# Kernel optimization log

Hardware: AMD Instinct MI355X
Metric: run time of the kernel (lower is better)

Reference implementation:

```python
import jax, jax.numpy as jnp
import numpy as np

N = 50000; E = 1600000; W = 12; CIN = 32; CMID = 32; COUT = 32; K = 2; KER = 3; DIL = 1


def setup_inputs() -> dict:
    key = jax.random.key(0)
    ks = jax.random.split(key, 6)
    x = jax.random.normal(ks[0], (W, N, CIN), jnp.float32)
    A = jax.random.randint(ks[1], (2, E), 0, N, jnp.int32)
    Ew = jax.random.uniform(ks[2], (E,), jnp.float32)
    Wcheb = jax.random.normal(ks[3], (W, K, CIN, CMID), jnp.float32) / np.sqrt(CIN)
    bcheb = jnp.zeros((W, CMID), jnp.float32)
    Wconv = jax.random.normal(ks[4], (COUT, CMID, KER), jnp.float32) / np.sqrt(CMID * KER)
    bconv = jnp.zeros((COUT,), jnp.float32)
    return dict(x=x, A=A, Ew=Ew, Wcheb=Wcheb, bcheb=bcheb, Wconv=Wconv, bconv=bconv, batch_size=1)


def _prop(x, src, dst, w_hat):
    # one sparse matvec with L_hat per timestep; x: [W, N, C]
    msg = x[:, src, :] * w_hat[None, :, None]                      # [W, E, C]
    agg = jax.ops.segment_sum(msg.transpose(1, 0, 2), dst, num_segments=x.shape[1])  # [N, W, C]
    return agg.transpose(1, 0, 2)                                  # [W, N, C]


def reference(x, A, Ew, Wcheb, bcheb, Wconv, bconv, batch_size):
    src, dst = A[0], A[1]
    # sym-normalized Laplacian with lambda_max=2: L_hat = -D^{-1/2} A D^{-1/2}
    deg = jax.ops.segment_sum(Ew, dst, num_segments=x.shape[1])
    dinv = jnp.where(deg > 0, jax.lax.rsqrt(jnp.maximum(deg, 1e-12)), 0.0)
    w_hat = -dinv[src] * Ew * dinv[dst]

    # Chebyshev recurrence (vectorized over all window_size graphs at once)
    Txs = [x, _prop(x, src, dst, w_hat)]
    for _ in range(Wcheb.shape[1] - 2):
        Txs.append(2.0 * _prop(Txs[-1], src, dst, w_hat) - Txs[-2])

    out = bcheb[:, None, :]                                        # [W, 1, CMID]
    for k, Txk in enumerate(Txs):
        out = out + jnp.einsum('wnc,wcd->wnd', Txk, Wcheb[:, k])   # per-timestep weights

    # temporal Conv1d over the window axis: nodes act as conv batch
    h = out.transpose(1, 2, 0)                                     # [N, CMID, W]
    pad = (KER // 2) * DIL
    h = jax.lax.conv_general_dilated(h, Wconv, (1,), [(pad, pad)], rhs_dilation=(DIL,),
                                     dimension_numbers=('NCH', 'OIH', 'NCH'))
    h = h + bconv[None, :, None]
    h = h.transpose(0, 2, 1)                                       # [N, W, COUT]
    h = jnp.where(h >= 0, h, 0.01 * h)                             # LeakyReLU; dropout p=0 is identity
    return h
```

## Files before the change

kernel.cpp:

```cpp
#include <hip/hip_runtime.h>

#define WW 12
#define CH 32
#define KERN 3
#define SBT 256
#define ROWB 384

typedef __attribute__((ext_vector_type(8))) short short8v;
typedef __attribute__((ext_vector_type(4))) short short4v;
typedef __attribute__((ext_vector_type(4))) float f32x4;

__device__ __forceinline__ unsigned short bf16rne(float v) {
  unsigned int u = __float_as_uint(v);
  return (unsigned short)((u + 0x7FFFu + ((u >> 16) & 1u)) >> 16);
}
__device__ __forceinline__ float bf16tof(unsigned int b) {
  return __uint_as_float(b << 16);
}

__device__ __forceinline__ unsigned char fp8e4m3(float x) {
  unsigned int u = __float_as_uint(x);
  unsigned int s = (u >> 24) & 0x80u;
  float ax = fabsf(x);
  if (ax >= 464.f) return (unsigned char)(s | 0x7E);
  if (ax < 0.015625f) {
    int m = __float2int_rn(ax * 512.f);
    return (unsigned char)(s | (unsigned)m);
  }
  unsigned int au = u & 0x7fffffffu;
  au += 0x7FFFFu + ((au >> 20) & 1u);
  int e = (int)(au >> 23) - 127 + 7;
  unsigned int m = (au >> 20) & 7u;
  if (e > 15 || (e == 15 && m == 7)) return (unsigned char)(s | 0x7E);
  return (unsigned char)(s | ((unsigned)e << 3) | m);
}

__device__ __forceinline__ void dec4fma(unsigned int u, float wh, float* acc) {
#if __has_builtin(__builtin_amdgcn_cvt_pk_f32_fp8)
  auto lo = __builtin_amdgcn_cvt_pk_f32_fp8((int)u, false);
  auto hi = __builtin_amdgcn_cvt_pk_f32_fp8((int)u, true);
  acc[0] = fmaf(wh, lo[0], acc[0]);
  acc[1] = fmaf(wh, lo[1], acc[1]);
  acc[2] = fmaf(wh, hi[0], acc[2]);
  acc[3] = fmaf(wh, hi[1], acc[3]);
#else
#pragma unroll
  for (int j = 0; j < 4; ++j) {
    unsigned int b = (u >> (8 * j)) & 0xffu;
    float f = __uint_as_float(((b & 0x80u) << 24) | ((b & 0x7fu) << 20)) * 0x1.0p120f;
    acc[j] = fmaf(wh, f, acc[j]);
  }
#endif
}

__global__ void rankpack_kernel(const int* __restrict__ dst, const float* __restrict__ Ew,
                                unsigned long long* __restrict__ degcnt,
                                unsigned short* __restrict__ rank,
                                const float* __restrict__ x, const float* __restrict__ Wcheb,
                                const float* __restrict__ Wconv,
                                unsigned short* __restrict__ xt, unsigned char* __restrict__ xq,
                                unsigned short* __restrict__ wb01, unsigned short* __restrict__ wbc,
                                int E, int N, int npackTot, int npx) {
  const int group = blockIdx.x / 7;
  const int slot = blockIdx.x % 7;
  if (slot == 6) {
    int base = group * 1024 + threadIdx.x;
#pragma unroll
    for (int u = 0; u < 4; ++u) {
      int e = base + u * 256;
      if (e < E) {
        unsigned int q = (unsigned int)__float2int_rn(Ew[e] * 33554432.f);
        unsigned long long old =
            atomicAdd(&degcnt[dst[e]], (1ULL << 32) | (unsigned long long)q);
        rank[e] = (unsigned short)(old >> 32);
      }
    }
    return;
  }
  int pid = group * 6 + slot;
  if (pid >= npackTot) return;
  if (pid < npx) {
    long long f = ((long long)pid * 256 + threadIdx.x) * 8;
    const long long T = (long long)WW * N * CH;
    if (f >= T) return;
    float4 v0 = *(const float4*)(x + f);
    float4 v1 = *(const float4*)(x + f + 4);
    int w = (int)(f / ((long long)N * CH));
    int rem = (int)(f - (long long)w * N * CH);
    int n = rem >> 5;
    int c = rem & 31;
    size_t o = (size_t)n * ROWB + w * CH + c;
    short4v h0, h1;
    h0[0] = (short)bf16rne(v0.x); h0[1] = (short)bf16rne(v0.y);
    h0[2] = (short)bf16rne(v0.z); h0[3] = (short)bf16rne(v0.w);
    h1[0] = (short)bf16rne(v1.x); h1[1] = (short)bf16rne(v1.y);
    h1[2] = (short)bf16rne(v1.z); h1[3] = (short)bf16rne(v1.w);
    *(short4v*)(xt + o) = h0;
    *(short4v*)(xt + o + 4) = h1;
    unsigned int q0 = (unsigned int)fp8e4m3(v0.x) | ((unsigned int)fp8e4m3(v0.y) << 8) |
                      ((unsigned int)fp8e4m3(v0.z) << 16) | ((unsigned int)fp8e4m3(v0.w) << 24);
    unsigned int q1 = (unsigned int)fp8e4m3(v1.x) | ((unsigned int)fp8e4m3(v1.y) << 8) |
                      ((unsigned int)fp8e4m3(v1.z) << 16) | ((unsigned int)fp8e4m3(v1.w) << 24);
    *(unsigned int*)(xq + o) = q0;
    *(unsigned int*)(xq + o + 4) = q1;
    return;
  }
  int id = (pid - npx) * 256 + threadIdx.x;
  if (id < 12 * 2 * 2 * 64 * 8) {
    int j = id & 7, l = (id >> 3) & 63, h = (id >> 9) & 1, m = (id >> 10) & 1, ww = id >> 11;
    int k = ((l >> 4) << 3) + j;
    int d = (l & 15) + (h << 4);
    wb01[id] = bf16rne(Wcheb[((size_t)(ww * 2 + m) * 32 + k) * 32 + d]);
  } else if (id < 24576 + 3 * 2 * 64 * 8) {
    int i2 = id - 24576;
    int j = i2 & 7, l = (i2 >> 3) & 63, h = (i2 >> 9) & 1, k = i2 >> 10;
    int c = ((l >> 4) << 3) + j;
    int o = (l & 15) + (h << 4);
    wbc[i2] = bf16rne(Wconv[((size_t)(o * 32 + c)) * 3 + k]);
  }
}

__global__ void scanA_kernel(const unsigned long long* __restrict__ degcnt,
                             int* __restrict__ bsum, int N) {
  __shared__ int red[SBT];
  int i = blockIdx.x * SBT + threadIdx.x;
  red[threadIdx.x] = (i < N) ? (int)(degcnt[i] >> 32) : 0;
  __syncthreads();
  for (int o = SBT / 2; o > 0; o >>= 1) {
    if (threadIdx.x < o) red[threadIdx.x] += red[threadIdx.x + o];
    __syncthreads();
  }
  if (threadIdx.x == 0) bsum[blockIdx.x] = red[0];
}

__global__ void scanB_kernel(int* __restrict__ bsum, int* __restrict__ rowptr,
                             int nb, int N) {
  __shared__ int tmp[SBT];
  int tid = threadIdx.x;
  int v = (tid < nb) ? bsum[tid] : 0;
  tmp[tid] = v;
  __syncthreads();
  for (int o = 1; o < SBT; o <<= 1) {
    int t = (tid >= o) ? tmp[tid - o] : 0;
    __syncthreads();
    tmp[tid] += t;
    __syncthreads();
  }
  if (tid < nb) bsum[tid] = tmp[tid] - v;
  if (tid == SBT - 1) rowptr[N] = tmp[SBT - 1];
}

__global__ void scanC_kernel(const unsigned long long* __restrict__ degcnt,
                             const int* __restrict__ bsum,
                             int* __restrict__ rowptr, int N) {
  __shared__ int tmp[SBT];
  int tid = threadIdx.x;
  int i = blockIdx.x * SBT + tid;
  int v = (i < N) ? (int)(degcnt[i] >> 32) : 0;
  tmp[tid] = v;
  __syncthreads();
  for (int o = 1; o < SBT; o <<= 1) {
    int t = (tid >= o) ? tmp[tid - o] : 0;
    __syncthreads();
    tmp[tid] += t;
    __syncthreads();
  }
  if (i < N) rowptr[i] = bsum[blockIdx.x] + tmp[tid] - v;
}

__global__ void fill_kernel(const int* __restrict__ src, const int* __restrict__ dst,
                            const float* __restrict__ Ew,
                            const unsigned long long* __restrict__ degcnt,
                            const int* __restrict__ rowptr,
                            const unsigned short* __restrict__ rank,
                            unsigned int* __restrict__ epair, int E) {
  int e = blockIdx.x * blockDim.x + threadIdx.x;
  if (e < E) {
    int s = src[e], d = dst[e];
    float ds = (float)(unsigned int)degcnt[s] * (1.f / 33554432.f);
    float dd = (float)(unsigned int)degcnt[d] * (1.f / 33554432.f);
    float is = (ds > 0.f) ? rsqrtf(fmaxf(ds, 1e-12f)) : 0.f;
    float id_ = (dd > 0.f) ? rsqrtf(fmaxf(dd, 1e-12f)) : 0.f;
    float wh = -is * Ew[e] * id_;
    int pos = rowptr[d] + rank[e];
    epair[pos] = ((unsigned int)s << 16) | bf16rne(wh);
  }
}

__global__ __launch_bounds__(256) void gather_kernel(
    const int* __restrict__ rowptr, const unsigned int* __restrict__ epair,
    const unsigned char* __restrict__ xq, unsigned short* __restrict__ zt, int N) {
  int gt = blockIdx.x * blockDim.x + threadIdx.x;
  int n = gt >> 6;
  if (n >= N) return;
  int lane = gt & 63;
  int half = lane >> 5;
  int l = lane & 31;

  float acc[WW];
#pragma unroll
  for (int j = 0; j < WW; ++j) acc[j] = 0.f;

  int i = rowptr[n] + half;
  const int i1 = rowptr[n + 1];
  for (; i + 6 < i1; i += 8) {
    unsigned int e0 = epair[i];
    unsigned int e1 = epair[i + 2];
    unsigned int e2 = epair[i + 4];
    unsigned int e3 = epair[i + 6];
    const unsigned int* p0 = (const unsigned int*)(xq + (size_t)(e0 >> 16) * ROWB + l * 12);
    const unsigned int* p1 = (const unsigned int*)(xq + (size_t)(e1 >> 16) * ROWB + l * 12);
    const unsigned int* p2 = (const unsigned int*)(xq + (size_t)(e2 >> 16) * ROWB + l * 12);
    const unsigned int* p3 = (const unsigned int*)(xq + (size_t)(e3 >> 16) * ROWB + l * 12);
    unsigned int a0 = p0[0], a1 = p0[1], a2 = p0[2];
    unsigned int b0 = p1[0], b1 = p1[1], b2 = p1[2];
    unsigned int c0 = p2[0], c1 = p2[1], c2 = p2[2];
    unsigned int d0 = p3[0], d1 = p3[1], d2 = p3[2];
    float w0 = bf16tof(e0 & 0xffffu);
    float w1 = bf16tof(e1 & 0xffffu);
    float w2 = bf16tof(e2 & 0xffffu);
    float w3 = bf16tof(e3 & 0xffffu);
    dec4fma(a0, w0, acc + 0); dec4fma(a1, w0, acc + 4); dec4fma(a2, w0, acc + 8);
    dec4fma(b0, w1, acc + 0); dec4fma(b1, w1, acc + 4); dec4fma(b2, w1, acc + 8);
    dec4fma(c0, w2, acc + 0); dec4fma(c1, w2, acc + 4); dec4fma(c2, w2, acc + 8);
    dec4fma(d0, w3, acc + 0); dec4fma(d1, w3, acc + 4); dec4fma(d2, w3, acc + 8);
  }
  for (; i < i1; i += 2) {
    unsigned int e0 = epair[i];
    const unsigned int* p0 = (const unsigned int*)(xq + (size_t)(e0 >> 16) * ROWB + l * 12);
    unsigned int a0 = p0[0], a1 = p0[1], a2 = p0[2];
    float w0 = bf16tof(e0 & 0xffffu);
    dec4fma(a0, w0, acc + 0); dec4fma(a1, w0, acc + 4); dec4fma(a2, w0, acc + 8);
  }
#pragma unroll
  for (int j = 0; j < WW; ++j) acc[j] += __shfl_xor(acc[j], 32);

  if (half == 0) {
    unsigned short* q = zt + (size_t)n * ROWB + l * 12;
    short4v o0, o1, o2;
#pragma unroll
    for (int j = 0; j < 4; ++j) {
      o0[j] = (short)bf16rne(acc[j]);
      o1[j] = (short)bf16rne(acc[4 + j]);
      o2[j] = (short)bf16rne(acc[8 + j]);
    }
    *(short4v*)(q) = o0;
    *(short4v*)(q + 4) = o1;
    *(short4v*)(q + 8) = o2;
  }
}

__global__ __launch_bounds__(256) void mc_kernel(
    const unsigned short* __restrict__ xt, const unsigned short* __restrict__ zt,
    const unsigned short* __restrict__ wb01, const unsigned short* __restrict__ wbc,
    const float* __restrict__ bcheb, const float* __restrict__ bconv,
    float* __restrict__ out, int N) {
  __shared__ __align__(16) unsigned short hts[4][4][16][40];
  const int wid = threadIdx.x >> 6;
  const int lane = threadIdx.x & 63;
  const int n0 = (blockIdx.x * 4 + wid) * 16;
  if (n0 >= N) return;
  const int kg = lane >> 4;
  const int arow = lane & 15;
  const int rrow = min(n0 + arow, N - 1);

  short8v wcf0[3], wcf1[3];
#pragma unroll
  for (int k = 0; k < 3; ++k) {
    wcf0[k] = *(const short8v*)(wbc + (((k * 2 + 0) * 64 + lane) << 3));
    wcf1[k] = *(const short8v*)(wbc + (((k * 2 + 1) * 64 + lane) << 3));
  }
  const float bc0 = bconv[arow];
  const float bc1 = bconv[arow + 16];

  auto computeH = [&](int w) {
    const size_t fofs = (size_t)rrow * ROWB + w * CH + kg * 8;
    short8v xf = *(const short8v*)(xt + fofs);
    short8v zf = *(const short8v*)(zt + fofs);
    unsigned short* hrow = &hts[wid][w & 3][0][0];
#pragma unroll
    for (int h = 0; h < 2; ++h) {
      short8v w0f = *(const short8v*)(wb01 + ((((w * 2 + 0) * 2 + h) * 64 + lane) << 3));
      short8v w1f = *(const short8v*)(wb01 + ((((w * 2 + 1) * 2 + h) * 64 + lane) << 3));
      f32x4 acc = {0.f, 0.f, 0.f, 0.f};
      acc = __builtin_amdgcn_mfma_f32_16x16x32_bf16(xf, w0f, acc, 0, 0, 0);
      acc = __builtin_amdgcn_mfma_f32_16x16x32_bf16(zf, w1f, acc, 0, 0, 0);
      const int d = arow + (h << 4);
      const float bias = bcheb[w * CH + d];
#pragma unroll
      for (int r = 0; r < 4; ++r) {
        hrow[(kg * 4 + r) * 40 + d] = bf16rne(acc[r] + bias);
      }
    }
  };

  auto convT = [&](int t) {
    f32x4 a0 = {0.f, 0.f, 0.f, 0.f};
    f32x4 a1 = {0.f, 0.f, 0.f, 0.f};
#pragma unroll
    for (int k = 0; k < 3; ++k) {
      int w = t + k - 1;
      if (w < 0 || w >= WW) continue;
      short8v hf = *(const short8v*)(&hts[wid][w & 3][arow][kg * 8]);
      a0 = __builtin_amdgcn_mfma_f32_16x16x32_bf16(hf, wcf0[k], a0, 0, 0, 0);
      a1 = __builtin_amdgcn_mfma_f32_16x16x32_bf16(hf, wcf1[k], a1, 0, 0, 0);
    }
#pragma unroll
    for (int r = 0; r < 4; ++r) {
      int node = n0 + kg * 4 + r;
      if (node >= N) continue;
      float v0 = a0[r] + bc0;
      float v1 = a1[r] + bc1;
      v0 = (v0 >= 0.f) ? v0 : 0.01f * v0;
      v1 = (v1 >= 0.f) ? v1 : 0.01f * v1;
      size_t o = ((size_t)node * WW + t) * CH;
      out[o + arow] = v0;
      out[o + arow + 16] = v1;
    }
  };

  computeH(0);
  computeH(1);
  convT(0);
  for (int w = 2; w < WW; ++w) {
    computeH(w);
    convT(w - 1);
  }
  convT(WW - 1);
}

extern "C" void kernel_launch(void* const* d_in, const int* in_sizes, int n_in,
                              void* d_out, int out_size, void* d_ws, size_t ws_size,
                              hipStream_t stream) {
  const float* x     = (const float*)d_in[0];
  const int*   A     = (const int*)d_in[1];
  const float* Ew    = (const float*)d_in[2];
  const float* Wcheb = (const float*)d_in[3];
  const float* bcheb = (const float*)d_in[4];
  const float* Wconv = (const float*)d_in[5];
  const float* bconv = (const float*)d_in[6];
  float* out = (float*)d_out;

  const int E = in_sizes[2];
  const int N = in_sizes[0] / (WW * CH);
  const int* srcA = A;
  const int* dstA = A + E;

  char* ws = (char*)d_ws;
  size_t off = 0;
  auto alloc = [&](size_t bytes) -> void* {
    void* p = ws + off;
    off += (bytes + 255) / 256 * 256;
    return p;
  };
  unsigned long long* degcnt = (unsigned long long*)alloc((size_t)N * 8);
  int*   rowptr = (int*)alloc((size_t)(N + 1) * 4);
  int*   bsum   = (int*)alloc((size_t)SBT * 4);
  unsigned short* rank = (unsigned short*)alloc((size_t)E * 2);
  unsigned int* epair = (unsigned int*)alloc((size_t)E * 4);
  unsigned short* xt   = (unsigned short*)alloc((size_t)N * ROWB * 2);
  unsigned char*  xq   = (unsigned char*)alloc((size_t)N * ROWB);
  unsigned short* zt   = (unsigned short*)alloc((size_t)N * ROWB * 2);
  unsigned short* wb01 = (unsigned short*)alloc((size_t)24576 * 2);
  unsigned short* wbc  = (unsigned short*)alloc((size_t)3072 * 2);
  (void)ws_size;

  hipMemsetAsync(degcnt, 0, (size_t)N * 8, stream);

  const long long T = (long long)WW * N * CH;
  const int npx = (int)((T + 2047) / 2048);
  const int nwb = (24576 + 3072 + 255) / 256;
  const int npackTot = npx + nwb;
  const int nbR = (E + 1023) / 1024;
  const int ngroups = max(nbR, (npackTot + 5) / 6);
  rankpack_kernel<<<ngroups * 7, 256, 0, stream>>>(
      dstA, Ew, degcnt, rank, x, Wcheb, Wconv, xt, xq, wb01, wbc, E, N, npackTot, npx);

  const int nb = (N + SBT - 1) / SBT;
  scanA_kernel<<<nb, SBT, 0, stream>>>(degcnt, bsum, N);
  scanB_kernel<<<1, SBT, 0, stream>>>(bsum, rowptr, nb, N);
  scanC_kernel<<<nb, SBT, 0, stream>>>(degcnt, bsum, rowptr, N);

  fill_kernel<<<(E + 255) / 256, 256, 0, stream>>>(srcA, dstA, Ew, degcnt, rowptr, rank, epair, E);

  long long gtot = (long long)N * 64;
  gather_kernel<<<(unsigned)((gtot + 255) / 256), 256, 0, stream>>>(rowptr, epair, xq, zt, N);

  int ntiles = (N + 15) / 16;
  int mcblocks = (ntiles + 3) / 4;
  mc_kernel<<<mcblocks, 256, 0, stream>>>(xt, zt, wb01, wbc, bcheb, bconv, out, N);
}
```

Before: 249.7 us.

## Privatize degree-count atomics into eight slices and precompute dinv per node

The degree/count atomics in the edge-counting pass are spread over eight slice copies of the counter array, chosen by edge block. This is meant to reduce atomic contention on hot destination nodes. The scan kernels merge the slices into per-node counts, compute dinv once per node, and build per-slice CSR offsets so that fill can still place each edge. In exchange there is a larger memset, more scan-side reads and an extra sliceoff array, and the order of edges within a row changes.

```diff
diff --git a/kernel.cpp b/kernel.cpp
--- a/kernel.cpp
+++ b/kernel.cpp
@@ -5,6 +5,7 @@
 #define KERN 3
 #define SBT 256
 #define ROWB 384
+#define NSL 8
 
 typedef __attribute__((ext_vector_type(8))) short short8v;
 typedef __attribute__((ext_vector_type(4))) short short4v;
@@ -54,7 +55,7 @@
 }
 
 __global__ void rankpack_kernel(const int* __restrict__ dst, const float* __restrict__ Ew,
-                                unsigned long long* __restrict__ degcnt,
+                                unsigned long long* __restrict__ degcnt8,
                                 unsigned short* __restrict__ rank,
                                 const float* __restrict__ x, const float* __restrict__ Wcheb,
                                 const float* __restrict__ Wconv,
@@ -69,9 +70,10 @@
     for (int u = 0; u < 4; ++u) {
       int e = base + u * 256;
       if (e < E) {
+        int slice = (group * 4 + u) & (NSL - 1);
         unsigned int q = (unsigned int)__float2int_rn(Ew[e] * 33554432.f);
-        unsigned long long old =
-            atomicAdd(&degcnt[dst[e]], (1ULL << 32) | (unsigned long long)q);
+        unsigned long long old = atomicAdd(&degcnt8[(size_t)slice * N + dst[e]],
+                                           (1ULL << 32) | (unsigned long long)q);
         rank[e] = (unsigned short)(old >> 32);
       }
     }
@@ -120,11 +122,25 @@
   }
 }
 
-__global__ void scanA_kernel(const unsigned long long* __restrict__ degcnt,
-                             int* __restrict__ bsum, int N) {
+__global__ void scanA_kernel(const unsigned long long* __restrict__ degcnt8,
+                             int* __restrict__ bsum, int* __restrict__ ncnt,
+                             float* __restrict__ dinv, int N) {
   __shared__ int red[SBT];
   int i = blockIdx.x * SBT + threadIdx.x;
-  red[threadIdx.x] = (i < N) ? (int)(degcnt[i] >> 32) : 0;
+  int c = 0;
+  if (i < N) {
+    unsigned int wsum = 0;
+#pragma unroll
+    for (int s = 0; s < NSL; ++s) {
+      unsigned long long v = degcnt8[(size_t)s * N + i];
+      c += (int)(v >> 32);
+      wsum += (unsigned int)v;
+    }
+    ncnt[i] = c;
+    float deg = (float)wsum * (1.f / 33554432.f);
+    dinv[i] = (deg > 0.f) ? rsqrtf(fmaxf(deg, 1e-12f)) : 0.f;
+  }
+  red[threadIdx.x] = c;
   __syncthreads();
   for (int o = SBT / 2; o > 0; o >>= 1) {
     if (threadIdx.x < o) red[threadIdx.x] += red[threadIdx.x + o];
@@ -150,13 +166,13 @@
   if (tid == SBT - 1) rowptr[N] = tmp[SBT - 1];
 }
 
-__global__ void scanC_kernel(const unsigned long long* __restrict__ degcnt,
-                             const int* __restrict__ bsum,
-                             int* __restrict__ rowptr, int N) {
+__global__ void scanC_kernel(const unsigned long long* __restrict__ degcnt8,
+                             const int* __restrict__ bsum, const int* __restrict__ ncnt,
+                             int* __restrict__ rowptr, int* __restrict__ sliceoff, int N) {
   __shared__ int tmp[SBT];
   int tid = threadIdx.x;
   int i = blockIdx.x * SBT + tid;
-  int v = (i < N) ? (int)(degcnt[i] >> 32) : 0;
+  int v = (i < N) ? ncnt[i] : 0;
   tmp[tid] = v;
   __syncthreads();
   for (int o = 1; o < SBT; o <<= 1) {
@@ -165,24 +181,29 @@
     tmp[tid] += t;
     __syncthreads();
   }
-  if (i < N) rowptr[i] = bsum[blockIdx.x] + tmp[tid] - v;
+  if (i < N) {
+    int ex = bsum[blockIdx.x] + tmp[tid] - v;
+    rowptr[i] = ex;
+    int run = ex;
+#pragma unroll
+    for (int s = 0; s < NSL; ++s) {
+      sliceoff[(size_t)s * N + i] = run;
+      run += (int)(degcnt8[(size_t)s * N + i] >> 32);
+    }
+  }
 }
 
 __global__ void fill_kernel(const int* __restrict__ src, const int* __restrict__ dst,
-                            const float* __restrict__ Ew,
-                            const unsigned long long* __restrict__ degcnt,
-                            const int* __restrict__ rowptr,
+                            const float* __restrict__ Ew, const float* __restrict__ dinv,
+                            const int* __restrict__ sliceoff,
                             const unsigned short* __restrict__ rank,
-                            unsigned int* __restrict__ epair, int E) {
+                            unsigned int* __restrict__ epair, int E, int N) {
   int e = blockIdx.x * blockDim.x + threadIdx.x;
   if (e < E) {
     int s = src[e], d = dst[e];
-    float ds = (float)(unsigned int)degcnt[s] * (1.f / 33554432.f);
-    float dd = (float)(unsigned int)degcnt[d] * (1.f / 33554432.f);
-    float is = (ds > 0.f) ? rsqrtf(fmaxf(ds, 1e-12f)) : 0.f;
-    float id_ = (dd > 0.f) ? rsqrtf(fmaxf(dd, 1e-12f)) : 0.f;
-    float wh = -is * Ew[e] * id_;
-    int pos = rowptr[d] + rank[e];
+    int slice = (e >> 8) & (NSL - 1);
+    float wh = -dinv[s] * Ew[e] * dinv[d];
+    int pos = sliceoff[(size_t)slice * N + d] + rank[e];
     epair[pos] = ((unsigned int)s << 16) | bf16rne(wh);
   }
 }
@@ -353,9 +374,12 @@
     off += (bytes + 255) / 256 * 256;
     return p;
   };
-  unsigned long long* degcnt = (unsigned long long*)alloc((size_t)N * 8);
-  int*   rowptr = (int*)alloc((size_t)(N + 1) * 4);
-  int*   bsum   = (int*)alloc((size_t)SBT * 4);
+  unsigned long long* degcnt8 = (unsigned long long*)alloc((size_t)NSL * N * 8);
+  int*   rowptr  = (int*)alloc((size_t)(N + 1) * 4);
+  int*   bsum    = (int*)alloc((size_t)SBT * 4);
+  int*   ncnt    = (int*)alloc((size_t)N * 4);
+  float* dinv    = (float*)alloc((size_t)N * 4);
+  int*   sliceoff= (int*)alloc((size_t)NSL * N * 4);
   unsigned short* rank = (unsigned short*)alloc((size_t)E * 2);
   unsigned int* epair = (unsigned int*)alloc((size_t)E * 4);
   unsigned short* xt   = (unsigned short*)alloc((size_t)N * ROWB * 2);
@@ -365,7 +389,7 @@
   unsigned short* wbc  = (unsigned short*)alloc((size_t)3072 * 2);
   (void)ws_size;
 
-  hipMemsetAsync(degcnt, 0, (size_t)N * 8, stream);
+  hipMemsetAsync(degcnt8, 0, (size_t)NSL * N * 8, stream);
 
   const long long T = (long long)WW * N * CH;
   const int npx = (int)((T + 2047) / 2048);
@@ -374,14 +398,14 @@
   const int nbR = (E + 1023) / 1024;
   const int ngroups = max(nbR, (npackTot + 5) / 6);
   rankpack_kernel<<<ngroups * 7, 256, 0, stream>>>(
-      dstA, Ew, degcnt, rank, x, Wcheb, Wconv, xt, xq, wb01, wbc, E, N, npackTot, npx);
+      dstA, Ew, degcnt8, rank, x, Wcheb, Wconv, xt, xq, wb01, wbc, E, N, npackTot, npx);
 
   const int nb = (N + SBT - 1) / SBT;
-  scanA_kernel<<<nb, SBT, 0, stream>>>(degcnt, bsum, N);
+  scanA_kernel<<<nb, SBT, 0, stream>>>(degcnt8, bsum, ncnt, dinv, N);
   scanB_kernel<<<1, SBT, 0, stream>>>(bsum, rowptr, nb, N);
-  scanC_kernel<<<nb, SBT, 0, stream>>>(degcnt, bsum, rowptr, N);
-
-  fill_kernel<<<(E + 255) / 256, 256, 0, stream>>>(srcA, dstA, Ew, degcnt, rowptr, rank, epair, E);
+  scanC_kernel<<<nb, SBT, 0, stream>>>(degcnt8, bsum, ncnt, rowptr, sliceoff, N);
+
+  fill_kernel<<<(E + 255) / 256, 256, 0, stream>>>(srcA, dstA, Ew, dinv, sliceoff, rank, epair, E, N);
 
   long long gtot = (long long)N * 64;
   gather_kernel<<<(unsigned)((gtot + 255) / 256), 256, 0, stream>>>(rowptr, epair, xq, zt, N);
```

Result: no change. 250.7 us (+0.4%).

## Replace global-atomic CSR build with two-pass bucketed radix sort by destination

Applied to the files above, without the earlier changes.

Replaces the per-edge 64-bit global atomic degree/rank counting and the scatter fill with a two-pass LDS-histogram radix sort: edges are bucketed by dst>>8 into an intermediate 8-byte record array, then each bucket block computes local row offsets, degree sums and dinv and scatters the final epair entries. Normalization is moved into the gather kernel, which multiplies the raw bf16 edge weight by dinv of source and destination on the fly. The aim is to remove heavily contended global atomics and random scattered writes. In exchange it adds an extra pass over an E*8-byte buffer, extra dinv lookups in the hot gather loop, and it rounds the edge weight to bf16 before the degree sum is taken.

```diff
diff --git a/kernel.cpp b/kernel.cpp
--- a/kernel.cpp
+++ b/kernel.cpp
@@ -3,8 +3,8 @@
 #define WW 12
 #define CH 32
 #define KERN 3
-#define SBT 256
 #define ROWB 384
+#define EBLK 8192
 
 typedef __attribute__((ext_vector_type(8))) short short8v;
 typedef __attribute__((ext_vector_type(4))) short short4v;
@@ -53,31 +53,100 @@
 #endif
 }
 
-__global__ void rankpack_kernel(const int* __restrict__ dst, const float* __restrict__ Ew,
-                                unsigned long long* __restrict__ degcnt,
-                                unsigned short* __restrict__ rank,
-                                const float* __restrict__ x, const float* __restrict__ Wcheb,
-                                const float* __restrict__ Wconv,
-                                unsigned short* __restrict__ xt, unsigned char* __restrict__ xq,
-                                unsigned short* __restrict__ wb01, unsigned short* __restrict__ wbc,
-                                int E, int N, int npackTot, int npx) {
-  const int group = blockIdx.x / 7;
-  const int slot = blockIdx.x % 7;
-  if (slot == 6) {
-    int base = group * 1024 + threadIdx.x;
-#pragma unroll
-    for (int u = 0; u < 4; ++u) {
-      int e = base + u * 256;
+__global__ __launch_bounds__(256) void histA_kernel(const int* __restrict__ dst,
+                                                    int* __restrict__ blockhist,
+                                                    int E, int NB) {
+  __shared__ unsigned int hist[256];
+  const int b = blockIdx.x;
+  const int tid = threadIdx.x;
+  hist[tid] = 0;
+  __syncthreads();
+  const int base = b * EBLK;
+#pragma unroll
+  for (int k = 0; k < EBLK / 256; ++k) {
+    int e = base + k * 256 + tid;
+    if (e < E) atomicAdd(&hist[(unsigned)dst[e] >> 8], 1u);
+  }
+  __syncthreads();
+  blockhist[tid * NB + b] = (int)hist[tid];
+}
+
+__global__ void scanA_kernel(const int* __restrict__ in, int* __restrict__ bsum, int M) {
+  __shared__ int red[256];
+  int i = blockIdx.x * 256 + threadIdx.x;
+  red[threadIdx.x] = (i < M) ? in[i] : 0;
+  __syncthreads();
+  for (int o = 128; o > 0; o >>= 1) {
+    if (threadIdx.x < o) red[threadIdx.x] += red[threadIdx.x + o];
+    __syncthreads();
+  }
+  if (threadIdx.x == 0) bsum[blockIdx.x] = red[0];
+}
+__global__ void scanB_kernel(int* __restrict__ bsum, int nb) {
+  __shared__ int tmp[256];
+  int tid = threadIdx.x;
+  int v = (tid < nb) ? bsum[tid] : 0;
+  tmp[tid] = v;
+  __syncthreads();
+  for (int o = 1; o < 256; o <<= 1) {
+    int t = (tid >= o) ? tmp[tid - o] : 0;
+    __syncthreads();
+    tmp[tid] += t;
+    __syncthreads();
+  }
+  if (tid < nb) bsum[tid] = tmp[tid] - v;
+}
+__global__ void scanC_kernel(const int* __restrict__ in, const int* __restrict__ bsum,
+                             int* __restrict__ out, int M) {
+  __shared__ int tmp[256];
+  int tid = threadIdx.x;
+  int i = blockIdx.x * 256 + tid;
+  int v = (i < M) ? in[i] : 0;
+  tmp[tid] = v;
+  __syncthreads();
+  for (int o = 1; o < 256; o <<= 1) {
+    int t = (tid >= o) ? tmp[tid - o] : 0;
+    __syncthreads();
+    tmp[tid] += t;
+    __syncthreads();
+  }
+  if (i < M) out[i] = bsum[blockIdx.x] + tmp[tid] - v;
+}
+
+__global__ __launch_bounds__(256) void scatpack_kernel(
+    const int* __restrict__ src, const int* __restrict__ dst, const float* __restrict__ Ew,
+    const int* __restrict__ scanout, unsigned long long* __restrict__ rec8,
+    const float* __restrict__ x, const float* __restrict__ Wcheb,
+    const float* __restrict__ Wconv,
+    unsigned short* __restrict__ xt, unsigned char* __restrict__ xq,
+    unsigned short* __restrict__ wb01, unsigned short* __restrict__ wbc,
+    int E, int N, int NB, int npackTot, int npx) {
+  const int group = blockIdx.x / 49;
+  const int slot = blockIdx.x % 49;
+  if (slot == 48) {
+    const int b = group;
+    if (b >= NB) return;
+    __shared__ unsigned int hist[256];
+    const int tid = threadIdx.x;
+    hist[tid] = 0;
+    __syncthreads();
+    const int base = b * EBLK;
+#pragma unroll
+    for (int k = 0; k < EBLK / 256; ++k) {
+      int e = base + k * 256 + tid;
       if (e < E) {
-        unsigned int q = (unsigned int)__float2int_rn(Ew[e] * 33554432.f);
-        unsigned long long old =
-            atomicAdd(&degcnt[dst[e]], (1ULL << 32) | (unsigned long long)q);
-        rank[e] = (unsigned short)(old >> 32);
+        int d = dst[e];
+        int bucket = (unsigned)d >> 8;
+        unsigned int lr = atomicAdd(&hist[bucket], 1u);
+        int pos = scanout[bucket * NB + b] + (int)lr;
+        unsigned long long rec = ((unsigned long long)(unsigned)d << 32) |
+                                 ((unsigned)src[e] << 16) | bf16rne(Ew[e]);
+        rec8[pos] = rec;
       }
     }
     return;
   }
-  int pid = group * 6 + slot;
+  int pid = group * 48 + slot;
   if (pid >= npackTot) return;
   if (pid < npx) {
     long long f = ((long long)pid * 256 + threadIdx.x) * 8;
@@ -120,75 +189,59 @@
   }
 }
 
-__global__ void scanA_kernel(const unsigned long long* __restrict__ degcnt,
-                             int* __restrict__ bsum, int N) {
-  __shared__ int red[SBT];
-  int i = blockIdx.x * SBT + threadIdx.x;
-  red[threadIdx.x] = (i < N) ? (int)(degcnt[i] >> 32) : 0;
-  __syncthreads();
-  for (int o = SBT / 2; o > 0; o >>= 1) {
-    if (threadIdx.x < o) red[threadIdx.x] += red[threadIdx.x + o];
-    __syncthreads();
-  }
-  if (threadIdx.x == 0) bsum[blockIdx.x] = red[0];
-}
-
-__global__ void scanB_kernel(int* __restrict__ bsum, int* __restrict__ rowptr,
-                             int nb, int N) {
-  __shared__ int tmp[SBT];
-  int tid = threadIdx.x;
-  int v = (tid < nb) ? bsum[tid] : 0;
+__global__ __launch_bounds__(256) void passB_kernel(
+    const unsigned long long* __restrict__ rec8, const int* __restrict__ scanout,
+    int* __restrict__ rowptr, float* __restrict__ dinv,
+    unsigned int* __restrict__ epair, int N, int E, int NB) {
+  __shared__ unsigned int hist[256];
+  __shared__ unsigned int qsum[256];
+  __shared__ int sub[256];
+  __shared__ int tmp[256];
+  const int B = blockIdx.x;
+  const int tid = threadIdx.x;
+  hist[tid] = 0;
+  qsum[tid] = 0;
+  __syncthreads();
+  const int bstart = scanout[B * NB];
+  const int bend = scanout[(B + 1) * NB];
+  for (int i = bstart + tid; i < bend; i += 256) {
+    unsigned long long r = rec8[i];
+    int low = (int)((r >> 32) & 255u);
+    atomicAdd(&hist[low], 1u);
+    unsigned int q = (unsigned int)__float2int_rn(bf16tof((unsigned int)r & 0xffffu) * 16777216.f);
+    atomicAdd(&qsum[low], q);
+  }
+  __syncthreads();
+  int v = (int)hist[tid];
   tmp[tid] = v;
   __syncthreads();
-  for (int o = 1; o < SBT; o <<= 1) {
+  for (int o = 1; o < 256; o <<= 1) {
     int t = (tid >= o) ? tmp[tid - o] : 0;
     __syncthreads();
     tmp[tid] += t;
     __syncthreads();
   }
-  if (tid < nb) bsum[tid] = tmp[tid] - v;
-  if (tid == SBT - 1) rowptr[N] = tmp[SBT - 1];
-}
-
-__global__ void scanC_kernel(const unsigned long long* __restrict__ degcnt,
-                             const int* __restrict__ bsum,
-                             int* __restrict__ rowptr, int N) {
-  __shared__ int tmp[SBT];
-  int tid = threadIdx.x;
-  int i = blockIdx.x * SBT + tid;
-  int v = (i < N) ? (int)(degcnt[i] >> 32) : 0;
-  tmp[tid] = v;
-  __syncthreads();
-  for (int o = 1; o < SBT; o <<= 1) {
-    int t = (tid >= o) ? tmp[tid - o] : 0;
-    __syncthreads();
-    tmp[tid] += t;
-    __syncthreads();
-  }
-  if (i < N) rowptr[i] = bsum[blockIdx.x] + tmp[tid] - v;
-}
-
-__global__ void fill_kernel(const int* __restrict__ src, const int* __restrict__ dst,
-                            const float* __restrict__ Ew,
-                            const unsigned long long* __restrict__ degcnt,
-                            const int* __restrict__ rowptr,
-                            const unsigned short* __restrict__ rank,
-                            unsigned int* __restrict__ epair, int E) {
-  int e = blockIdx.x * blockDim.x + threadIdx.x;
-  if (e < E) {
-    int s = src[e], d = dst[e];
-    float ds = (float)(unsigned int)degcnt[s] * (1.f / 33554432.f);
-    float dd = (float)(unsigned int)degcnt[d] * (1.f / 33554432.f);
-    float is = (ds > 0.f) ? rsqrtf(fmaxf(ds, 1e-12f)) : 0.f;
-    float id_ = (dd > 0.f) ? rsqrtf(fmaxf(dd, 1e-12f)) : 0.f;
-    float wh = -is * Ew[e] * id_;
-    int pos = rowptr[d] + rank[e];
-    epair[pos] = ((unsigned int)s << 16) | bf16rne(wh);
+  sub[tid] = tmp[tid] - v;
+  int n = (B << 8) + tid;
+  if (n < N) {
+    rowptr[n] = bstart + sub[tid];
+    float deg = (float)qsum[tid] * (1.f / 16777216.f);
+    dinv[n] = (deg > 0.f) ? rsqrtf(fmaxf(deg, 1e-12f)) : 0.f;
+  }
+  if (B == 0 && tid == 0) rowptr[N] = E;
+  hist[tid] = 0;
+  __syncthreads();
+  for (int i = bstart + tid; i < bend; i += 256) {
+    unsigned long long r = rec8[i];
+    int low = (int)((r >> 32) & 255u);
+    unsigned int lr = atomicAdd(&hist[low], 1u);
+    epair[bstart + sub[low] + (int)lr] = (unsigned int)r;
   }
 }
 
 __global__ __launch_bounds__(256) void gather_kernel(
     const int* __restrict__ rowptr, const unsigned int* __restrict__ epair,
+    const float* __restrict__ dinv,
     const unsigned char* __restrict__ xq, unsigned short* __restrict__ zt, int N) {
   int gt = blockIdx.x * blockDim.x + threadIdx.x;
   int n = gt >> 6;
@@ -196,6 +249,8 @@
   int lane = gt & 63;
   int half = lane >> 5;
   int l = lane & 31;
+
+  const float ndinv = -dinv[n];
 
   float acc[WW];
 #pragma unroll
@@ -216,10 +271,10 @@
     unsigned int b0 = p1[0], b1 = p1[1], b2 = p1[2];
     unsigned int c0 = p2[0], c1 = p2[1], c2 = p2[2];
     unsigned int d0 = p3[0], d1 = p3[1], d2 = p3[2];
-    float w0 = bf16tof(e0 & 0xffffu);
-    float w1 = bf16tof(e1 & 0xffffu);
-    float w2 = bf16tof(e2 & 0xffffu);
-    float w3 = bf16tof(e3 & 0xffffu);
+    float w0 = ndinv * bf16tof(e0 & 0xffffu) * dinv[e0 >> 16];
+    float w1 = ndinv * bf16tof(e1 & 0xffffu) * dinv[e1 >> 16];
+    float w2 = ndinv * bf16tof(e2 & 0xffffu) * dinv[e2 >> 16];
+    float w3 = ndinv * bf16tof(e3 & 0xffffu) * dinv[e3 >> 16];
     dec4fma(a0, w0, acc + 0); dec4fma(a1, w0, acc + 4); dec4fma(a2, w0, acc + 8);
     dec4fma(b0, w1, acc + 0); dec4fma(b1, w1, acc + 4); dec4fma(b2, w1, acc + 8);
     dec4fma(c0, w2, acc + 0); dec4fma(c1, w2, acc + 4); dec4fma(c2, w2, acc + 8);
@@ -229,7 +284,7 @@
     unsigned int e0 = epair[i];
     const unsigned int* p0 = (const unsigned int*)(xq + (size_t)(e0 >> 16) * ROWB + l * 12);
     unsigned int a0 = p0[0], a1 = p0[1], a2 = p0[2];
-    float w0 = bf16tof(e0 & 0xffffu);
+    float w0 = ndinv * bf16tof(e0 & 0xffffu) * dinv[e0 >> 16];
     dec4fma(a0, w0, acc + 0); dec4fma(a1, w0, acc + 4); dec4fma(a2, w0, acc + 8);
   }
 #pragma unroll
@@ -353,10 +408,16 @@
     off += (bytes + 255) / 256 * 256;
     return p;
   };
-  unsigned long long* degcnt = (unsigned long long*)alloc((size_t)N * 8);
-  int*   rowptr = (int*)alloc((size_t)(N + 1) * 4);
-  int*   bsum   = (int*)alloc((size_t)SBT * 4);
-  unsigned short* rank = (unsigned short*)alloc((size_t)E * 2);
+  const int NB = (E + EBLK - 1) / EBLK;
+  const int M = 256 * NB;
+  const int NBUCK = (N + 255) / 256;
+
+  int* blockhist = (int*)alloc((size_t)M * 4);
+  int* scanout   = (int*)alloc((size_t)(M + 1) * 4);
+  int* bsum      = (int*)alloc((size_t)256 * 4);
+  int* rowptr    = (int*)alloc((size_t)(N + 1) * 4);
+  float* dinv    = (float*)alloc((size_t)N * 4);
+  unsigned long long* rec8 = (unsigned long long*)alloc((size_t)E * 8);
   unsigned int* epair = (unsigned int*)alloc((size_t)E * 4);
   unsigned short* xt   = (unsigned short*)alloc((size_t)N * ROWB * 2);
   unsigned char*  xq   = (unsigned char*)alloc((size_t)N * ROWB);
@@ -365,26 +426,26 @@
   unsigned short* wbc  = (unsigned short*)alloc((size_t)3072 * 2);
   (void)ws_size;
 
-  hipMemsetAsync(degcnt, 0, (size_t)N * 8, stream);
+  histA_kernel<<<NB, 256, 0, stream>>>(dstA, blockhist, E, NB);
+
+  const int nbs = (M + 255) / 256;
+  scanA_kernel<<<nbs, 256, 0, stream>>>(blockhist, bsum, M);
+  scanB_kernel<<<1, 256, 0, stream>>>(bsum, nbs);
+  scanC_kernel<<<nbs, 256, 0, stream>>>(blockhist, bsum, scanout, M);
 
   const long long T = (long long)WW * N * CH;
   const int npx = (int)((T + 2047) / 2048);
   const int nwb = (24576 + 3072 + 255) / 256;
   const int npackTot = npx + nwb;
-  const int nbR = (E + 1023) / 1024;
-  const int ngroups = max(nbR, (npackTot + 5) / 6);
-  rankpack_kernel<<<ngroups * 7, 256, 0, stream>>>(
-      dstA, Ew, degcnt, rank, x, Wcheb, Wconv, xt, xq, wb01, wbc, E, N, npackTot, npx);
-
-  const int nb = (N + SBT - 1) / SBT;
-  scanA_kernel<<<nb, SBT, 0, stream>>>(degcnt, bsum, N);
-  scanB_kernel<<<1, SBT, 0, stream>>>(bsum, rowptr, nb, N);
-  scanC_kernel<<<nb, SBT, 0, stream>>>(degcnt, bsum, rowptr, N);
-
-  fill_kernel<<<(E + 255) / 256, 256, 0, stream>>>(srcA, dstA, Ew, degcnt, rowptr, rank, epair, E);
+  const int ngroups = max(NB, (npackTot + 47) / 48);
+  scatpack_kernel<<<ngroups * 49, 256, 0, stream>>>(
+      srcA, dstA, Ew, scanout, rec8, x, Wcheb, Wconv, xt, xq, wb01, wbc,
+      E, N, NB, npackTot, npx);
+
+  passB_kernel<<<NBUCK, 256, 0, stream>>>(rec8, scanout, rowptr, dinv, epair, N, E, NB);
 
   long long gtot = (long long)N * 64;
-  gather_kernel<<<(unsigned)((gtot + 255) / 256), 256, 0, stream>>>(rowptr, epair, xq, zt, N);
+  gather_kernel<<<(unsigned)((gtot + 255) / 256), 256, 0, stream>>>(rowptr, epair, dinv, xq, zt, N);
 
   int ntiles = (N + 15) / 16;
   int mcblocks = (ntiles + 3) / 4;
```

Measured after the change: 253.0 us. Within noise of the previous version (+1.3%).
